# Optimization experiments

Measured on AMD Instinct MI355X. Metric: run time of the kernel, lower is better.

Reference implementation:

```python
import jax, jax.numpy as jnp
import numpy as np
import math

D_MODEL = 512
NHEAD = 8
D_K = D_MODEL // NHEAD
FACTOR = 5


def setup_inputs() -> dict:
    key = jax.random.key(0)
    ks = jax.random.split(key, 9)
    B, L = 2, 2048
    s = 1.0 / math.sqrt(D_MODEL)
    inp = {
        "x": jax.random.normal(ks[0], (B, L, D_MODEL), dtype=jnp.float32),
        "Wq": jax.random.normal(ks[1], (D_MODEL, D_MODEL), dtype=jnp.float32) * s,
        "bq": jnp.zeros((D_MODEL,), dtype=jnp.float32),
        "Wk": jax.random.normal(ks[2], (D_MODEL, D_MODEL), dtype=jnp.float32) * s,
        "bk": jnp.zeros((D_MODEL,), dtype=jnp.float32),
        "Wv": jax.random.normal(ks[3], (D_MODEL, D_MODEL), dtype=jnp.float32) * s,
        "bv": jnp.zeros((D_MODEL,), dtype=jnp.float32),
        "Wo": jax.random.normal(ks[4], (D_MODEL, D_MODEL), dtype=jnp.float32) * s,
        "bo": jnp.zeros((D_MODEL,), dtype=jnp.float32),
    }
    return inp


def reference(x, Wq, bq, Wk, bk, Wv, bv, Wo, bo):
    B, L, _ = x.shape
    # u keys kept per query (static: depends only on static L)
    u = min(L, int(FACTOR * math.log(L)) if L > 1 else L)

    def proj(W, b):
        # [B,L,D] -> [B,H,L,d_k]
        y = x @ W.T + b
        return y.reshape(B, L, NHEAD, D_K).transpose(0, 2, 1, 3)

    Q = proj(Wq, bq)
    K = proj(Wk, bk)
    V = proj(Wv, bv)

    scores = jnp.einsum("bhqd,bhkd->bhqk", Q, K) / math.sqrt(D_K)  # [B,H,L,L]
    # topk thresholding: keep only scores >= u-th largest per query row
    topk_vals, _ = jax.lax.top_k(scores, u)
    thresh = topk_vals[..., -1:]
    scores = jnp.where(scores < thresh, -10000.0, scores)
    attn = jax.nn.softmax(scores, axis=-1)  # dropout disabled (p=0 / eval)
    out = jnp.einsum("bhqk,bhkd->bhqd", attn, V)  # [B,H,L,d_k]
    out = out.transpose(0, 2, 1, 3).reshape(B, L, D_MODEL)
    return out @ Wo.T + bo
```

## Files before the change

### kernel.cpp

```cpp
#include <hip/hip_runtime.h>
#include <hip/hip_fp16.h>
#include <math.h>

#define LSEQ   2048
#define DMODEL 512
#define NHEAD  8
#define DK     64
#define UK     38

typedef __attribute__((ext_vector_type(8))) _Float16 v8h;
typedef __attribute__((ext_vector_type(4))) _Float16 v4h;
typedef __attribute__((ext_vector_type(4))) float    v4f;

__device__ __forceinline__ unsigned long long mapu64(double x){
    unsigned long long s = (unsigned long long)__double_as_longlong(x);
    return (s & 0x8000000000000000ull) ? ~s : (s | 0x8000000000000000ull);
}
__device__ __forceinline__ unsigned map32(float x){
    unsigned s = __float_as_uint(x);
    return (s & 0x80000000u) ? ~s : (s | 0x80000000u);
}
__device__ __forceinline__ float unmap32(unsigned u){
    unsigned s = (u & 0x80000000u) ? (u & 0x7fffffffu) : ~u;
    return __uint_as_float(s);
}
__device__ __forceinline__ unsigned map16(unsigned h){
    return (h & 0x8000u) ? ((~h) & 0xFFFFu) : (h | 0x8000u);
}

__global__ __launch_bounds__(256) void split_hl(
    const float* __restrict__ X,  const float* __restrict__ Wq,
    const float* __restrict__ Wk, const float* __restrict__ Wv,
    _Float16* __restrict__ Xh, _Float16* __restrict__ Xl,
    _Float16* __restrict__ Whl)
{
    const int idx = blockIdx.x * 256 + threadIdx.x;
    const int NXQ = (4096 * 512) / 4;
    const float* __restrict__ src;
    _Float16* __restrict__ dh;
    _Float16* __restrict__ dl;
    size_t off;
    if (idx < NXQ){
        src = X; dh = Xh; dl = Xl; off = (size_t)idx * 4;
    } else {
        int wi = idx - NXQ;
        int m  = wi >> 16;
        src = (m == 0) ? Wq : (m == 1 ? Wk : Wv);
        dh  = Whl + (size_t)m * 524288;
        dl  = dh + 262144;
        off = (size_t)(wi & 65535) * 4;
    }
    float4 v = *(const float4*)&src[off];
    v4h h, l;
    h[0] = (_Float16)v.x; l[0] = (_Float16)(v.x - (float)h[0]);
    h[1] = (_Float16)v.y; l[1] = (_Float16)(v.y - (float)h[1]);
    h[2] = (_Float16)v.z; l[2] = (_Float16)(v.z - (float)h[2]);
    h[3] = (_Float16)v.w; l[3] = (_Float16)(v.w - (float)h[3]);
    *(v4h*)&dh[off] = h;
    *(v4h*)&dl[off] = l;
}

__global__ __launch_bounds__(256) void qkv_f16(
    const _Float16* __restrict__ Xh, const _Float16* __restrict__ Xl,
    const _Float16* __restrict__ Whl,
    const float* __restrict__ bq, const float* __restrict__ bk,
    const float* __restrict__ bv,
    double* __restrict__ qD, double* __restrict__ kRow,
    __half* __restrict__ qH, __half* __restrict__ kH, float* __restrict__ vB)
{
    const int mode = blockIdx.z;
    const _Float16* __restrict__ Wh = Whl + (size_t)mode * 524288;
    const _Float16* __restrict__ Wl = Wh + 262144;
    const float* __restrict__ bias = (mode == 0) ? bq : (mode == 1 ? bk : bv);
    const int r0 = blockIdx.x * 64, c0 = blockIdx.y * 64;
    __shared__ _Float16 Ah[64][72], Al[64][72];
    __shared__ _Float16 Bh[64][72], Bl[64][72];
    const int tid  = threadIdx.x;
    const int lane = tid & 63, wv = tid >> 6;
    const int m0   = wv << 4;
    const int row  = lane & 15, kq = lane >> 4;

    v4f acc[4] = {};

    for (int kb = 0; kb < DMODEL; kb += 64){
        __syncthreads();
        #pragma unroll
        for (int it = 0; it < 2; ++it){
            int slot = it * 256 + tid;
            int m = slot >> 3, o8 = (slot & 7) << 3;
            size_t ga = (size_t)(r0 + m) * DMODEL + kb + o8;
            size_t gb = (size_t)(c0 + m) * DMODEL + kb + o8;
            *(v8h*)&Ah[m][o8] = *(const v8h*)&Xh[ga];
            *(v8h*)&Al[m][o8] = *(const v8h*)&Xl[ga];
            *(v8h*)&Bh[m][o8] = *(const v8h*)&Wh[gb];
            *(v8h*)&Bl[m][o8] = *(const v8h*)&Wl[gb];
        }
        __syncthreads();
        v8h ah0 = *(const v8h*)&Ah[m0 + row][kq * 8];
        v8h ah1 = *(const v8h*)&Ah[m0 + row][kq * 8 + 32];
        v8h al0 = *(const v8h*)&Al[m0 + row][kq * 8];
        v8h al1 = *(const v8h*)&Al[m0 + row][kq * 8 + 32];
        #pragma unroll
        for (int j = 0; j < 4; ++j){
            const int j0 = j << 4;
            v8h bh0 = *(const v8h*)&Bh[j0 + row][kq * 8];
            v8h bh1 = *(const v8h*)&Bh[j0 + row][kq * 8 + 32];
            v8h bl0 = *(const v8h*)&Bl[j0 + row][kq * 8];
            v8h bl1 = *(const v8h*)&Bl[j0 + row][kq * 8 + 32];
            acc[j] = __builtin_amdgcn_mfma_f32_16x16x32_f16(ah0, bh0, acc[j], 0, 0, 0);
            acc[j] = __builtin_amdgcn_mfma_f32_16x16x32_f16(ah0, bl0, acc[j], 0, 0, 0);
            acc[j] = __builtin_amdgcn_mfma_f32_16x16x32_f16(al0, bh0, acc[j], 0, 0, 0);
            acc[j] = __builtin_amdgcn_mfma_f32_16x16x32_f16(ah1, bh1, acc[j], 0, 0, 0);
            acc[j] = __builtin_amdgcn_mfma_f32_16x16x32_f16(ah1, bl1, acc[j], 0, 0, 0);
            acc[j] = __builtin_amdgcn_mfma_f32_16x16x32_f16(al1, bh1, acc[j], 0, 0, 0);
        }
    }

    const int h = c0 >> 6;
    #pragma unroll
    for (int j = 0; j < 4; ++j){
        const int dk = (j << 4) + row;
        const float bi = bias[c0 + dk];
        #pragma unroll
        for (int rr = 0; rr < 4; ++rr){
            const int r = r0 + m0 + (kq << 2) + rr;
            const int bidx = r >> 11, l = r & 2047;
            const size_t rowb = (size_t)(bidx * NHEAD + h) * LSEQ + l;
            float v = acc[j][rr] + bi;
            if (mode == 0){
                double vd = (double)v * 0.125;
                qD[rowb * DK + dk] = vd;
                ((_Float16*)qH)[rowb * DK + dk] = (_Float16)vd;
            } else if (mode == 1){
                kRow[rowb * DK + dk] = (double)v;
                ((_Float16*)kH)[rowb * DK + dk] = (_Float16)v;
            } else {
                vB[rowb * DK + dk] = v;
            }
        }
    }
}

__global__ __launch_bounds__(256) void gemm_f32(
    const float* __restrict__ X, const float* __restrict__ W,
    const float* __restrict__ bias, float* __restrict__ out)
{
    const int r0 = blockIdx.x * 64, c0 = blockIdx.y * 64;
    __shared__ float Xs[32][68];
    __shared__ float Ws[32][68];
    const int tid = threadIdx.x;
    const int tx = tid & 15, ty = tid >> 4;
    float acc[4][4] = {};
    for (int kb = 0; kb < DMODEL; kb += 32){
        __syncthreads();
        #pragma unroll
        for (int i = 0; i < 2; ++i){
            int f4 = i * 256 + tid;
            int m = f4 >> 3, kg = (f4 & 7) << 2;
            float4 xv = *(const float4*)&X[(r0 + m) * DMODEL + kb + kg];
            Xs[kg+0][m] = xv.x; Xs[kg+1][m] = xv.y; Xs[kg+2][m] = xv.z; Xs[kg+3][m] = xv.w;
            float4 wv = *(const float4*)&W[(c0 + m) * DMODEL + kb + kg];
            Ws[kg+0][m] = wv.x; Ws[kg+1][m] = wv.y; Ws[kg+2][m] = wv.z; Ws[kg+3][m] = wv.w;
        }
        __syncthreads();
        #pragma unroll
        for (int kk = 0; kk < 32; ++kk){
            float4 av = *(const float4*)&Xs[kk][ty << 2];
            float4 bv = *(const float4*)&Ws[kk][tx << 2];
            float a[4] = {av.x, av.y, av.z, av.w};
            float b[4] = {bv.x, bv.y, bv.z, bv.w};
            #pragma unroll
            for (int ii = 0; ii < 4; ++ii)
                #pragma unroll
                for (int jj = 0; jj < 4; ++jj)
                    acc[ii][jj] = fmaf(a[ii], b[jj], acc[ii][jj]);
        }
    }
    #pragma unroll
    for (int ii = 0; ii < 4; ++ii){
        int r = r0 + (ty << 2) + ii;
        float4 o;
        o.x = acc[ii][0] + bias[c0 + (tx << 2) + 0];
        o.y = acc[ii][1] + bias[c0 + (tx << 2) + 1];
        o.z = acc[ii][2] + bias[c0 + (tx << 2) + 2];
        o.w = acc[ii][3] + bias[c0 + (tx << 2) + 3];
        *(float4*)&out[(size_t)r * DMODEL + c0 + (tx << 2)] = o;
    }
}

__global__ __launch_bounds__(256) void score_gemm(
    const __half* __restrict__ qH, const __half* __restrict__ kH,
    __half* __restrict__ Sh, const int bh0)
{
    const int bh = bh0 + blockIdx.z;
    const int r0 = blockIdx.x * 64, c0 = blockIdx.y * 64;
    __shared__ _Float16 Qs[64][72];
    __shared__ _Float16 Ks[64][72];
    const int tid = threadIdx.x;
    const int lane = tid & 63, wv = tid >> 6;
    const size_t qb = ((size_t)bh * LSEQ + r0) * DK;
    const size_t kb = ((size_t)bh * LSEQ + c0) * DK;
    #pragma unroll
    for (int i = 0; i < 2; ++i){
        int c = i * 256 + tid;
        int m = c >> 3, off8 = (c & 7) << 3;
        *(v8h*)&Qs[m][off8] = *(const v8h*)&qH[qb + (size_t)m * DK + off8];
        *(v8h*)&Ks[m][off8] = *(const v8h*)&kH[kb + (size_t)m * DK + off8];
    }
    __syncthreads();
    const int m0 = wv << 4;
    const int row = lane & 15, kq = lane >> 4;
    v8h a0 = *(const v8h*)&Qs[m0 + row][kq * 8];
    v8h a1 = *(const v8h*)&Qs[m0 + row][kq * 8 + 32];
    #pragma unroll
    for (int j0 = 0; j0 < 64; j0 += 16){
        v8h b0 = *(const v8h*)&Ks[j0 + row][kq * 8];
        v8h b1 = *(const v8h*)&Ks[j0 + row][kq * 8 + 32];
        v4f acc = {0.f, 0.f, 0.f, 0.f};
        acc = __builtin_amdgcn_mfma_f32_16x16x32_f16(a0, b0, acc, 0, 0, 0);
        acc = __builtin_amdgcn_mfma_f32_16x16x32_f16(a1, b1, acc, 0, 0, 0);
        #pragma unroll
        for (int r = 0; r < 4; ++r){
            int gr = r0 + m0 + kq * 4 + r;
            int gc = c0 + j0 + row;
            Sh[((size_t)blockIdx.z * LSEQ + gr) * LSEQ + gc] = (__half)acc[r];
        }
    }
}

__device__ __forceinline__ void finish_common(
    const int ncand, const int gl, const int bh, const int lane,
    const double qd, const double* __restrict__ kRow, const float* __restrict__ vB,
    float* __restrict__ ctx, int* __restrict__ jlsR, float* __restrict__ wlsR,
    double* __restrict__ sLds)
{
    const unsigned long long mlt = (1ull << lane) - 1ull;
    if (lane >= ncand) jlsR[lane] = 0;
    if (lane < 4) jlsR[64 + lane] = 0;
    int myJ = jlsR[lane];

    double q8[8];
    #pragma unroll
    for (int k = 0; k < 8; ++k) q8[k] = __shfl(qd, (lane & 7) + (k << 3));
    const int grp = lane >> 3, dl = lane & 7;
    const size_t kb = (size_t)bh * LSEQ;
    for (int e0 = 0; e0 < ncand; e0 += 8){
        int j = jlsR[e0 + grp];
        const double* __restrict__ kr = &kRow[(kb + j) * DK + dl];
        double s = 0.0;
        #pragma unroll
        for (int k = 0; k < 8; ++k) s = fma(q8[k], kr[k << 3], s);
        s += __shfl_xor(s, 1); s += __shfl_xor(s, 2); s += __shfl_xor(s, 4);
        if (dl == 0) sLds[e0 + grp] = s;
    }
    double myS = (lane < ncand) ? sLds[lane] : -1.0e308;

    unsigned long long cu = (lane < ncand) ? mapu64(myS) : 0ull;
    unsigned long long T64 = 0ull;
    for (int bit = 63; bit >= 0; --bit){
        unsigned long long Tp = T64 | (1ull << bit);
        int c = __popcll(__ballot(cu >= Tp));
        if (c >= UK){ T64 = Tp; if (c == UK) break; }
    }
    const bool sel = (cu >= T64);

    double xm = sel ? myS : -1.0e308;
    #pragma unroll
    for (int off = 32; off; off >>= 1) xm = fmax(xm, __shfl_xor(xm, off));
    float w = sel ? expf((float)(myS - xm)) : 0.0f;
    float z = w;
    #pragma unroll
    for (int off = 32; off; off >>= 1) z += __shfl_xor(z, off);
    unsigned long long bm = __ballot(sel);
    int p = __popcll(bm & mlt);
    if (sel){ wlsR[p] = w; jlsR[p] = myJ; }
    const int cnt = __popcll(bm);
    const float invZ = 1.0f / z;

    if (lane >= cnt) wlsR[lane] = 0.0f;
    if (lane < 4){ wlsR[64 + lane] = 0.0f; jlsR[64 + lane] = 0; }

    const float* __restrict__ vsl = vB + (size_t)bh * (LSEQ * DK);
    float o = 0.0f;
    for (int e = 0; e < cnt; e += 4){
        float w0 = wlsR[e],   w1 = wlsR[e+1], w2 = wlsR[e+2], w3 = wlsR[e+3];
        int   j0 = jlsR[e],   j1 = jlsR[e+1], j2 = jlsR[e+2], j3 = jlsR[e+3];
        float v0 = vsl[(size_t)j0 * DK + lane];
        float v1 = vsl[(size_t)j1 * DK + lane];
        float v2 = vsl[(size_t)j2 * DK + lane];
        float v3 = vsl[(size_t)j3 * DK + lane];
        o = fmaf(w0, v0, o); o = fmaf(w1, v1, o);
        o = fmaf(w2, v2, o); o = fmaf(w3, v3, o);
    }
    ctx[((size_t)(bh >> 3) * LSEQ + gl) * DMODEL + (bh & 7) * DK + lane] = o * invZ;
}

__device__ __forceinline__ void finish_row_f32(
    float (&acc)[32], const int gl, const int bh, const int lane, const float margin,
    const double qd, const double* __restrict__ kRow, const float* __restrict__ vB,
    float* __restrict__ ctx, int* __restrict__ jlsR, float* __restrict__ wlsR,
    double* __restrict__ sLds)
{
    unsigned u[32];
    #pragma unroll
    for (int ch = 0; ch < 32; ++ch) u[ch] = map32(acc[ch]);
    unsigned T = 0u; int curc = 2048;
    for (int bit = 31; bit >= 0; --bit){
        unsigned Tp = T | (1u << bit);
        int c = 0;
        #pragma unroll
        for (int ch = 0; ch < 32; ++ch) c += __popcll(__ballot(u[ch] >= Tp));
        if (c >= UK){ T = Tp; curc = c; }
        if (curc <= 48) break;
    }
    const unsigned Tlo = map32(unmap32(T) - margin);
    const unsigned long long mlt = (1ull << lane) - 1ull;
    int base = 0;
    #pragma unroll
    for (int ch = 0; ch < 32; ++ch){
        bool sel = (u[ch] >= Tlo);
        unsigned long long bm = __ballot(sel);
        int p = base + __popcll(bm & mlt);
        if (sel && p < 64) jlsR[p] = (ch << 6) + lane;
        base += __popcll(bm);
    }
    const int ncand = base > 64 ? 64 : base;
    finish_common(ncand, gl, bh, lane, qd, kRow, vB, ctx, jlsR, wlsR, sLds);
}

__global__ __launch_bounds__(256) void select_kernel(
    const __half* __restrict__ Sh, const double* __restrict__ qD,
    const double* __restrict__ kRow, const float* __restrict__ vB,
    float* __restrict__ ctx, const int bh0)
{
    __shared__ int    jls[4][68];
    __shared__ float  wls[4][68];
    __shared__ double sds[4][64];
    const int tid = threadIdx.x, lane = tid & 63, wv = tid >> 6;
    const int rgS = blockIdx.x * 4 + wv;
    const int bh = bh0 + (rgS >> 11), l = rgS & 2047;
    const double qd = qD[((size_t)bh * LSEQ + l) * DK + lane];
    unsigned u[32];
    const unsigned short* __restrict__ Srow =
        (const unsigned short*)Sh + (size_t)rgS * LSEQ;
    #pragma unroll
    for (int it = 0; it < 4; ++it){
        uint4 v = *(const uint4*)&Srow[it * 512 + (lane << 3)];
        unsigned ws[4] = {v.x, v.y, v.z, v.w};
        #pragma unroll
        for (int q = 0; q < 4; ++q){
            u[it*8 + 2*q]     = map16(ws[q] & 0xFFFFu);
            u[it*8 + 2*q + 1] = map16(ws[q] >> 16);
        }
    }
    unsigned T = 0u; int curc = 2048;
    for (int bit = 15; bit >= 0; --bit){
        unsigned Tp = T | (1u << bit);
        int c = 0;
        #pragma unroll
        for (int ch = 0; ch < 32; ++ch) c += __popcll(__ballot(u[ch] >= Tp));
        if (c >= UK){ T = Tp; curc = c; }
        if (curc <= 48) break;
    }
    unsigned hb = (T & 0x8000u) ? (T & 0x7FFFu) : ((~T) & 0xFFFFu);
    float tf = __half2float(__ushort_as_half((unsigned short)hb)) - 2.2e-2f;
    unsigned short tlb = __half_as_ushort(__float2half_rd(tf));
    const unsigned Tlo = map16(tlb);

    const unsigned long long mlt = (1ull << lane) - 1ull;
    int base = 0;
    #pragma unroll
    for (int ch = 0; ch < 32; ++ch){
        bool sel = (u[ch] >= Tlo);
        unsigned long long bm = __ballot(sel);
        int p = base + __popcll(bm & mlt);
        int j = ((ch >> 3) << 9) + (lane << 3) + (ch & 7);
        if (sel && p < 64) jls[wv][p] = j;
        base += __popcll(bm);
    }
    const int ncand = base > 64 ? 64 : base;
    finish_common(ncand, l, bh, lane, qd, kRow, vB, ctx,
                  &jls[wv][0], &wls[wv][0], &sds[wv][0]);
}

__global__ __launch_bounds__(256) void attn_kernel(
    const double* __restrict__ qD, const double* __restrict__ kRow,
    const float* __restrict__ vB, float* __restrict__ ctx)
{
    __shared__ float2 Kld2[16 * 66];
    __shared__ float  qsf[8][64];
    __shared__ int    jls[8][68];
    __shared__ float  wlsf[8][68];
    __shared__ double sds[8][64];

    const int tid = threadIdx.x, lane = tid & 63, wv = tid >> 6;
    const int bh = blockIdx.x >> 8;
    const int l0 = (blockIdx.x & 255) << 3;
    const int rA = l0 + (wv << 1), rB = rA + 1;

    for (int e = tid; e < 512; e += 256){
        int r = e >> 6, d = e & 63;
        qsf[r][d] = (float)qD[((size_t)bh * LSEQ + l0 + r) * DK + d];
    }
    const double qdA = qD[((size_t)bh * LSEQ + rA) * DK + lane];
    const double qdB = qD[((size_t)bh * LSEQ + rB) * DK + lane];

    float accA[32] = {}, accB[32] = {};
    const size_t kBase = (size_t)bh * (LSEQ * DK);

    for (int dh = 0; dh < 2; ++dh){
        __syncthreads();
        float qa[32], qb[32];
        #pragma unroll
        for (int i = 0; i < 8; ++i){
            float4 va = *(const float4*)&qsf[wv << 1][dh * 32 + i * 4];
            qa[i*4+0]=va.x; qa[i*4+1]=va.y; qa[i*4+2]=va.z; qa[i*4+3]=va.w;
            float4 vb4 = *(const float4*)&qsf[(wv << 1) + 1][dh * 32 + i * 4];
            qb[i*4+0]=vb4.x; qb[i*4+1]=vb4.y; qb[i*4+2]=vb4.z; qb[i*4+3]=vb4.w;
        }
        #pragma unroll
        for (int ch = 0; ch < 32; ++ch){
            const int cb = ch << 6;
            __syncthreads();
            #pragma unroll
            for (int i = 0; i < 4; ++i){
                int j   = i * 16 + (wv << 2) + (lane >> 4);
                int dpl = lane & 15;
                double2 kd = *(const double2*)&kRow[kBase + (size_t)(cb + j) * DK + dh * 32 + dpl * 2];
                Kld2[dpl * 66 + j] = make_float2((float)kd.x, (float)kd.y);
            }
            __syncthreads();
            float a0 = accA[ch], b0 = accB[ch];
            #pragma unroll
            for (int dpl = 0; dpl < 16; ++dpl){
                float2 k = Kld2[dpl * 66 + lane];
                a0 = fmaf(qa[2*dpl],   k.x, a0);
                a0 = fmaf(qa[2*dpl+1], k.y, a0);
                b0 = fmaf(qb[2*dpl],   k.x, b0);
                b0 = fmaf(qb[2*dpl+1], k.y, b0);
            }
            accA[ch] = a0; accB[ch] = b0;
        }
    }

    finish_row_f32(accA, rA, bh, lane, 1e-3f, qdA, kRow, vB, ctx,
                   &jls[wv<<1][0], &wlsf[wv<<1][0], &sds[wv<<1][0]);
    finish_row_f32(accB, rB, bh, lane, 1e-3f, qdB, kRow, vB, ctx,
                   &jls[(wv<<1)+1][0], &wlsf[(wv<<1)+1][0], &sds[(wv<<1)+1][0]);
}

extern "C" void kernel_launch(void* const* d_in, const int* in_sizes, int n_in,
                              void* d_out, int out_size, void* d_ws, size_t ws_size,
                              hipStream_t stream)
{
    const float* x  = (const float*)d_in[0];
    const float* Wq = (const float*)d_in[1];
    const float* bq = (const float*)d_in[2];
    const float* Wk = (const float*)d_in[3];
    const float* bk = (const float*)d_in[4];
    const float* Wv = (const float*)d_in[5];
    const float* bv = (const float*)d_in[6];
    const float* Wo = (const float*)d_in[7];
    const float* bo = (const float*)d_in[8];
    float* out = (float*)d_out;
    char* ws = (char*)d_ws;
    const size_t MiB = 1024 * 1024;
    double* qD   = (double*)(ws);
    double* kRow = (double*)(ws + 16 * MiB);
    float*  vB   = (float*) (ws + 32 * MiB);
    float*  ctx  = (float*) (ws + 40 * MiB);
    __half* qH   = (__half*)(ws + 48 * MiB);
    __half* kH   = (__half*)(ws + 52 * MiB);
    __half* Sh   = (__half*)(ws + 56 * MiB);
    _Float16* Xh  = (_Float16*)(ws + 40 * MiB);
    _Float16* Xl  = (_Float16*)(ws + 44 * MiB);
    _Float16* Whl = (_Float16*)(ws + 56 * MiB);
    size_t avail = (ws_size > 56 * MiB) ? (ws_size - 56 * MiB) : 0;
    int slab = (int)(avail / (8 * MiB)); if (slab > 16) slab = 16;

    dim3 blk(256);
    split_hl<<<dim3(2816), blk, 0, stream>>>(x, Wq, Wk, Wv, Xh, Xl, Whl);
    qkv_f16 <<<dim3(64, 8, 3), blk, 0, stream>>>(Xh, Xl, Whl, bq, bk, bv,
                                                 qD, kRow, qH, kH, vB);
    if (slab >= 1){
        for (int s0 = 0; s0 < NHEAD * 2; s0 += slab){
            int nb = NHEAD * 2 - s0; if (nb > slab) nb = slab;
            score_gemm   <<<dim3(32, 32, nb), blk, 0, stream>>>(qH, kH, Sh, s0);
            select_kernel<<<dim3(nb * 512),   blk, 0, stream>>>(Sh, qD, kRow, vB, ctx, s0);
        }
    } else {
        attn_kernel<<<dim3(4096), blk, 0, stream>>>(qD, kRow, vB, ctx);
    }
    gemm_f32<<<dim3(64, 8), blk, 0, stream>>>(ctx, Wo, bo, out);
}
```

Before: 271.1 us.

## Process two query rows per wave in select kernel and pre-map score keys

```diff
diff --git a/kernel.cpp b/kernel.cpp
--- a/kernel.cpp
+++ b/kernel.cpp
@@ -223,7 +223,9 @@
         for (int r = 0; r < 4; ++r){
             int gr = r0 + m0 + kq * 4 + r;
             int gc = c0 + j0 + row;
-            Sh[((size_t)blockIdx.z * LSEQ + gr) * LSEQ + gc] = (__half)acc[r];
+            unsigned hbits = (unsigned)__half_as_ushort((__half)acc[r]);
+            unsigned short key = (unsigned short)map16(hbits);
+            ((unsigned short*)Sh)[((size_t)blockIdx.z * LSEQ + gr) * LSEQ + gc] = key;
         }
     }
 }
@@ -328,59 +330,231 @@
     finish_common(ncand, gl, bh, lane, qd, kRow, vB, ctx, jlsR, wlsR, sLds);
 }
 
+__device__ __forceinline__ void finish2(
+    const int ncA, const int ncB, const int glA, const int glB,
+    const int bh, const int lane,
+    const double* __restrict__ qD, const double* __restrict__ kRow,
+    const float* __restrict__ vB, float* __restrict__ ctx,
+    int* __restrict__ jA, float* __restrict__ wA, double* __restrict__ sdA,
+    int* __restrict__ jB, float* __restrict__ wB, double* __restrict__ sdB)
+{
+    const unsigned long long mlt = (1ull << lane) - 1ull;
+    if (lane >= ncA) jA[lane] = 0;
+    if (lane >= ncB) jB[lane] = 0;
+    if (lane < 4){ jA[64 + lane] = 0; jB[64 + lane] = 0; }
+    const int myJA = jA[lane], myJB = jB[lane];
+
+    const int grp = lane >> 3, dl = lane & 7;
+    const size_t kb = (size_t)bh * LSEQ;
+
+    double q8A[8], q8B[8];
+    {
+        const double* __restrict__ qrA = qD + (kb + glA) * DK + dl;
+        const double* __restrict__ qrB = qD + (kb + glB) * DK + dl;
+        #pragma unroll
+        for (int k = 0; k < 8; ++k){ q8A[k] = qrA[k << 3]; q8B[k] = qrB[k << 3]; }
+    }
+
+    const int pNA = (ncA + 7) >> 3, pNB = (ncB + 7) >> 3;
+    const int pN = pNA > pNB ? pNA : pNB;
+    for (int p = 0; p < pN; ++p){
+        double kvA[8], kvB[8];
+        const bool doA = (p < pNA), doB = (p < pNB);
+        if (doA){
+            int j = jA[(p << 3) + grp];
+            const double* __restrict__ kr = &kRow[(kb + j) * DK + dl];
+            #pragma unroll
+            for (int k = 0; k < 8; ++k) kvA[k] = kr[k << 3];
+        }
+        if (doB){
+            int j = jB[(p << 3) + grp];
+            const double* __restrict__ kr = &kRow[(kb + j) * DK + dl];
+            #pragma unroll
+            for (int k = 0; k < 8; ++k) kvB[k] = kr[k << 3];
+        }
+        double sA = 0.0, sB = 0.0;
+        if (doA){
+            #pragma unroll
+            for (int k = 0; k < 8; ++k) sA = fma(q8A[k], kvA[k], sA);
+        }
+        if (doB){
+            #pragma unroll
+            for (int k = 0; k < 8; ++k) sB = fma(q8B[k], kvB[k], sB);
+        }
+        sA += __shfl_xor(sA, 1); sB += __shfl_xor(sB, 1);
+        sA += __shfl_xor(sA, 2); sB += __shfl_xor(sB, 2);
+        sA += __shfl_xor(sA, 4); sB += __shfl_xor(sB, 4);
+        if (dl == 0){
+            if (doA) sdA[(p << 3) + grp] = sA;
+            if (doB) sdB[(p << 3) + grp] = sB;
+        }
+    }
+    const double mySA = (lane < ncA) ? sdA[lane] : -1.0e308;
+    const double mySB = (lane < ncB) ? sdB[lane] : -1.0e308;
+
+    const unsigned long long cuA = (lane < ncA) ? mapu64(mySA) : 0ull;
+    const unsigned long long cuB = (lane < ncB) ? mapu64(mySB) : 0ull;
+    unsigned long long TA = 0ull, TB = 0ull;
+    bool dA = false, dB = false;
+    for (int bit = 63; bit >= 0; --bit){
+        if (!dA){
+            unsigned long long Tp = TA | (1ull << bit);
+            int c = __popcll(__ballot(cuA >= Tp));
+            if (c >= UK){ TA = Tp; if (c == UK) dA = true; }
+        }
+        if (!dB){
+            unsigned long long Tp = TB | (1ull << bit);
+            int c = __popcll(__ballot(cuB >= Tp));
+            if (c >= UK){ TB = Tp; if (c == UK) dB = true; }
+        }
+        if (dA && dB) break;
+    }
+    const bool selA = (cuA >= TA), selB = (cuB >= TB);
+
+    double xmA = selA ? mySA : -1.0e308, xmB = selB ? mySB : -1.0e308;
+    #pragma unroll
+    for (int off = 32; off; off >>= 1){
+        xmA = fmax(xmA, __shfl_xor(xmA, off));
+        xmB = fmax(xmB, __shfl_xor(xmB, off));
+    }
+    float wvA = selA ? expf((float)(mySA - xmA)) : 0.0f;
+    float wvB = selB ? expf((float)(mySB - xmB)) : 0.0f;
+    float zA = wvA, zB = wvB;
+    #pragma unroll
+    for (int off = 32; off; off >>= 1){
+        zA += __shfl_xor(zA, off);
+        zB += __shfl_xor(zB, off);
+    }
+    const unsigned long long bmA = __ballot(selA), bmB = __ballot(selB);
+    const int pA = __popcll(bmA & mlt), pB = __popcll(bmB & mlt);
+    if (selA){ wA[pA] = wvA; jA[pA] = myJA; }
+    if (selB){ wB[pB] = wvB; jB[pB] = myJB; }
+    const int cntA = __popcll(bmA), cntB = __popcll(bmB);
+    const float invZA = 1.0f / zA, invZB = 1.0f / zB;
+
+    if (lane >= cntA) wA[lane] = 0.0f;
+    if (lane >= cntB) wB[lane] = 0.0f;
+    if (lane < 4){ wA[64 + lane] = 0.0f; jA[64 + lane] = 0;
+                   wB[64 + lane] = 0.0f; jB[64 + lane] = 0; }
+
+    const float* __restrict__ vsl = vB + (size_t)bh * (LSEQ * DK);
+    float oA = 0.0f, oB = 0.0f;
+    const int emax = cntA > cntB ? cntA : cntB;
+    for (int e0 = 0; e0 < emax; e0 += 16){
+        float wa16[16], va16[16]; int ja16[16];
+        float wb16[16], vb16[16]; int jb16[16];
+        const bool gA = (e0 < cntA), gB = (e0 < cntB);
+        if (gA){
+            #pragma unroll
+            for (int t = 0; t < 16; ++t){ wa16[t] = wA[e0 + t]; ja16[t] = jA[e0 + t]; }
+        }
+        if (gB){
+            #pragma unroll
+            for (int t = 0; t < 16; ++t){ wb16[t] = wB[e0 + t]; jb16[t] = jB[e0 + t]; }
+        }
+        if (gA){
+            #pragma unroll
+            for (int t = 0; t < 16; ++t) va16[t] = vsl[(size_t)ja16[t] * DK + lane];
+        }
+        if (gB){
+            #pragma unroll
+            for (int t = 0; t < 16; ++t) vb16[t] = vsl[(size_t)jb16[t] * DK + lane];
+        }
+        if (gA){
+            #pragma unroll
+            for (int t = 0; t < 16; ++t) oA = fmaf(wa16[t], va16[t], oA);
+        }
+        if (gB){
+            #pragma unroll
+            for (int t = 0; t < 16; ++t) oB = fmaf(wb16[t], vb16[t], oB);
+        }
+    }
+    const size_t cb = (size_t)(bh >> 3) * LSEQ;
+    const int hc = (bh & 7) * DK + lane;
+    ctx[(cb + glA) * DMODEL + hc] = oA * invZA;
+    ctx[(cb + glB) * DMODEL + hc] = oB * invZB;
+}
+
 __global__ __launch_bounds__(256) void select_kernel(
     const __half* __restrict__ Sh, const double* __restrict__ qD,
     const double* __restrict__ kRow, const float* __restrict__ vB,
     float* __restrict__ ctx, const int bh0)
 {
-    __shared__ int    jls[4][68];
-    __shared__ float  wls[4][68];
-    __shared__ double sds[4][64];
+    __shared__ int    jls[8][68];
+    __shared__ float  wls[8][68];
+    __shared__ double sds[8][64];
     const int tid = threadIdx.x, lane = tid & 63, wv = tid >> 6;
-    const int rgS = blockIdx.x * 4 + wv;
-    const int bh = bh0 + (rgS >> 11), l = rgS & 2047;
-    const double qd = qD[((size_t)bh * LSEQ + l) * DK + lane];
-    unsigned u[32];
-    const unsigned short* __restrict__ Srow =
-        (const unsigned short*)Sh + (size_t)rgS * LSEQ;
+    const int base = blockIdx.x * 8 + (wv << 1);
+    const int rA = base, rB = base + 1;
+    const int bh = bh0 + (rA >> 11);
+    const int glA = rA & 2047, glB = rB & 2047;
+
+    const unsigned short* __restrict__ SrA =
+        (const unsigned short*)Sh + (size_t)rA * LSEQ;
+    const unsigned short* __restrict__ SrB =
+        (const unsigned short*)Sh + (size_t)rB * LSEQ;
+    uint4 la[4], lb[4];
     #pragma unroll
     for (int it = 0; it < 4; ++it){
-        uint4 v = *(const uint4*)&Srow[it * 512 + (lane << 3)];
-        unsigned ws[4] = {v.x, v.y, v.z, v.w};
+        la[it] = *(const uint4*)&SrA[it * 512 + (lane << 3)];
+        lb[it] = *(const uint4*)&SrB[it * 512 + (lane << 3)];
+    }
+    unsigned uA[32], uB[32];
+    #pragma unroll
+    for (int it = 0; it < 4; ++it){
+        unsigned wsA[4] = {la[it].x, la[it].y, la[it].z, la[it].w};
+        unsigned wsB[4] = {lb[it].x, lb[it].y, lb[it].z, lb[it].w};
         #pragma unroll
         for (int q = 0; q < 4; ++q){
-            u[it*8 + 2*q]     = map16(ws[q] & 0xFFFFu);
-            u[it*8 + 2*q + 1] = map16(ws[q] >> 16);
-        }
-    }
-    unsigned T = 0u; int curc = 2048;
+            uA[it*8 + 2*q]     = wsA[q] & 0xFFFFu;
+            uA[it*8 + 2*q + 1] = wsA[q] >> 16;
+            uB[it*8 + 2*q]     = wsB[q] & 0xFFFFu;
+            uB[it*8 + 2*q + 1] = wsB[q] >> 16;
+        }
+    }
+
+    unsigned TA = 0u, TB = 0u;
     for (int bit = 15; bit >= 0; --bit){
-        unsigned Tp = T | (1u << bit);
-        int c = 0;
-        #pragma unroll
-        for (int ch = 0; ch < 32; ++ch) c += __popcll(__ballot(u[ch] >= Tp));
-        if (c >= UK){ T = Tp; curc = c; }
-        if (curc <= 48) break;
-    }
-    unsigned hb = (T & 0x8000u) ? (T & 0x7FFFu) : ((~T) & 0xFFFFu);
-    float tf = __half2float(__ushort_as_half((unsigned short)hb)) - 2.2e-2f;
-    unsigned short tlb = __half_as_ushort(__float2half_rd(tf));
-    const unsigned Tlo = map16(tlb);
+        const unsigned TpA = TA | (1u << bit), TpB = TB | (1u << bit);
+        int cA = 0, cB = 0;
+        #pragma unroll
+        for (int ch = 0; ch < 32; ++ch){
+            cA += __popcll(__ballot(uA[ch] >= TpA));
+            cB += __popcll(__ballot(uB[ch] >= TpB));
+        }
+        if (cA >= UK) TA = TpA;
+        if (cB >= UK) TB = TpB;
+    }
+    unsigned hbA = (TA & 0x8000u) ? (TA & 0x7FFFu) : ((~TA) & 0xFFFFu);
+    unsigned hbB = (TB & 0x8000u) ? (TB & 0x7FFFu) : ((~TB) & 0xFFFFu);
+    float tfA = __half2float(__ushort_as_half((unsigned short)hbA)) - 2.2e-2f;
+    float tfB = __half2float(__ushort_as_half((unsigned short)hbB)) - 2.2e-2f;
+    const unsigned TloA = map16(__half_as_ushort(__float2half_rd(tfA)));
+    const unsigned TloB = map16(__half_as_ushort(__float2half_rd(tfB)));
 
     const unsigned long long mlt = (1ull << lane) - 1ull;
-    int base = 0;
+    int baseA = 0, baseB = 0;
+    int* __restrict__ jA = &jls[wv << 1][0];
+    int* __restrict__ jB = &jls[(wv << 1) + 1][0];
     #pragma unroll
     for (int ch = 0; ch < 32; ++ch){
-        bool sel = (u[ch] >= Tlo);
-        unsigned long long bm = __ballot(sel);
-        int p = base + __popcll(bm & mlt);
-        int j = ((ch >> 3) << 9) + (lane << 3) + (ch & 7);
-        if (sel && p < 64) jls[wv][p] = j;
-        base += __popcll(bm);
-    }
-    const int ncand = base > 64 ? 64 : base;
-    finish_common(ncand, l, bh, lane, qd, kRow, vB, ctx,
-                  &jls[wv][0], &wls[wv][0], &sds[wv][0]);
+        const int j = ((ch >> 3) << 9) + (lane << 3) + (ch & 7);
+        const bool sA = (uA[ch] >= TloA);
+        const bool sB = (uB[ch] >= TloB);
+        const unsigned long long bmA = __ballot(sA);
+        const unsigned long long bmB = __ballot(sB);
+        const int pA = baseA + __popcll(bmA & mlt);
+        const int pB = baseB + __popcll(bmB & mlt);
+        if (sA && pA < 64) jA[pA] = j;
+        if (sB && pB < 64) jB[pB] = j;
+        baseA += __popcll(bmA);
+        baseB += __popcll(bmB);
+    }
+    const int ncA = baseA > 64 ? 64 : baseA;
+    const int ncB = baseB > 64 ? 64 : baseB;
+    finish2(ncA, ncB, glA, glB, bh, lane, qD, kRow, vB, ctx,
+            jA, &wls[wv << 1][0], &sds[wv << 1][0],
+            jB, &wls[(wv << 1) + 1][0], &sds[(wv << 1) + 1][0]);
 }
 
 __global__ __launch_bounds__(256) void attn_kernel(
@@ -486,7 +660,7 @@
         for (int s0 = 0; s0 < NHEAD * 2; s0 += slab){
             int nb = NHEAD * 2 - s0; if (nb > slab) nb = slab;
             score_gemm   <<<dim3(32, 32, nb), blk, 0, stream>>>(qH, kH, Sh, s0);
-            select_kernel<<<dim3(nb * 512),   blk, 0, stream>>>(Sh, qD, kRow, vB, ctx, s0);
+            select_kernel<<<dim3(nb * 256),   blk, 0, stream>>>(Sh, qD, kRow, vB, ctx, s0);
         }
     } else {
         attn_kernel<<<dim3(4096), blk, 0, stream>>>(qD, kRow, vB, ctx);
```

Measured after the change: 309.6 us. +14.2%, slower.

## Compute scores in split-fp16 precision and skip double-precision refinement when threshold is clear

Applied to the files above, without the earlier changes.

```diff
diff --git a/kernel.cpp b/kernel.cpp
--- a/kernel.cpp
+++ b/kernel.cpp
@@ -23,9 +23,6 @@
 __device__ __forceinline__ float unmap32(unsigned u){
     unsigned s = (u & 0x80000000u) ? (u & 0x7fffffffu) : ~u;
     return __uint_as_float(s);
-}
-__device__ __forceinline__ unsigned map16(unsigned h){
-    return (h & 0x8000u) ? ((~h) & 0xFFFFu) : (h | 0x8000u);
 }
 
 __global__ __launch_bounds__(256) void split_hl(
@@ -66,7 +63,9 @@
     const float* __restrict__ bq, const float* __restrict__ bk,
     const float* __restrict__ bv,
     double* __restrict__ qD, double* __restrict__ kRow,
-    __half* __restrict__ qH, __half* __restrict__ kH, float* __restrict__ vB)
+    _Float16* __restrict__ qH, _Float16* __restrict__ kH,
+    _Float16* __restrict__ qL, _Float16* __restrict__ kL,
+    float* __restrict__ vB)
 {
     const int mode = blockIdx.z;
     const _Float16* __restrict__ Wh = Whl + (size_t)mode * 524288;
@@ -130,10 +129,15 @@
             if (mode == 0){
                 double vd = (double)v * 0.125;
                 qD[rowb * DK + dk] = vd;
-                ((_Float16*)qH)[rowb * DK + dk] = (_Float16)vd;
+                float sf = (float)vd;
+                _Float16 hi = (_Float16)sf;
+                qH[rowb * DK + dk] = hi;
+                qL[rowb * DK + dk] = (_Float16)(sf - (float)hi);
             } else if (mode == 1){
                 kRow[rowb * DK + dk] = (double)v;
-                ((_Float16*)kH)[rowb * DK + dk] = (_Float16)v;
+                _Float16 hi = (_Float16)v;
+                kH[rowb * DK + dk] = hi;
+                kL[rowb * DK + dk] = (_Float16)(v - (float)hi);
             } else {
                 vB[rowb * DK + dk] = v;
             }
@@ -189,13 +193,14 @@
 }
 
 __global__ __launch_bounds__(256) void score_gemm(
-    const __half* __restrict__ qH, const __half* __restrict__ kH,
-    __half* __restrict__ Sh, const int bh0)
+    const _Float16* __restrict__ qH, const _Float16* __restrict__ qL,
+    const _Float16* __restrict__ kH, const _Float16* __restrict__ kL,
+    unsigned* __restrict__ Sk, const int bh0)
 {
     const int bh = bh0 + blockIdx.z;
     const int r0 = blockIdx.x * 64, c0 = blockIdx.y * 64;
-    __shared__ _Float16 Qs[64][72];
-    __shared__ _Float16 Ks[64][72];
+    __shared__ _Float16 Qh[64][72], Ql[64][72];
+    __shared__ _Float16 Kh[64][72], Kl[64][72];
     const int tid = threadIdx.x;
     const int lane = tid & 63, wv = tid >> 6;
     const size_t qb = ((size_t)bh * LSEQ + r0) * DK;
@@ -204,26 +209,38 @@
     for (int i = 0; i < 2; ++i){
         int c = i * 256 + tid;
         int m = c >> 3, off8 = (c & 7) << 3;
-        *(v8h*)&Qs[m][off8] = *(const v8h*)&qH[qb + (size_t)m * DK + off8];
-        *(v8h*)&Ks[m][off8] = *(const v8h*)&kH[kb + (size_t)m * DK + off8];
+        size_t qa = qb + (size_t)m * DK + off8;
+        size_t ka = kb + (size_t)m * DK + off8;
+        *(v8h*)&Qh[m][off8] = *(const v8h*)&qH[qa];
+        *(v8h*)&Ql[m][off8] = *(const v8h*)&qL[qa];
+        *(v8h*)&Kh[m][off8] = *(const v8h*)&kH[ka];
+        *(v8h*)&Kl[m][off8] = *(const v8h*)&kL[ka];
     }
     __syncthreads();
     const int m0 = wv << 4;
     const int row = lane & 15, kq = lane >> 4;
-    v8h a0 = *(const v8h*)&Qs[m0 + row][kq * 8];
-    v8h a1 = *(const v8h*)&Qs[m0 + row][kq * 8 + 32];
+    v8h a0h = *(const v8h*)&Qh[m0 + row][kq * 8];
+    v8h a1h = *(const v8h*)&Qh[m0 + row][kq * 8 + 32];
+    v8h a0l = *(const v8h*)&Ql[m0 + row][kq * 8];
+    v8h a1l = *(const v8h*)&Ql[m0 + row][kq * 8 + 32];
     #pragma unroll
     for (int j0 = 0; j0 < 64; j0 += 16){
-        v8h b0 = *(const v8h*)&Ks[j0 + row][kq * 8];
-        v8h b1 = *(const v8h*)&Ks[j0 + row][kq * 8 + 32];
+        v8h b0h = *(const v8h*)&Kh[j0 + row][kq * 8];
+        v8h b1h = *(const v8h*)&Kh[j0 + row][kq * 8 + 32];
+        v8h b0l = *(const v8h*)&Kl[j0 + row][kq * 8];
+        v8h b1l = *(const v8h*)&Kl[j0 + row][kq * 8 + 32];
         v4f acc = {0.f, 0.f, 0.f, 0.f};
-        acc = __builtin_amdgcn_mfma_f32_16x16x32_f16(a0, b0, acc, 0, 0, 0);
-        acc = __builtin_amdgcn_mfma_f32_16x16x32_f16(a1, b1, acc, 0, 0, 0);
+        acc = __builtin_amdgcn_mfma_f32_16x16x32_f16(a0h, b0l, acc, 0, 0, 0);
+        acc = __builtin_amdgcn_mfma_f32_16x16x32_f16(a1h, b1l, acc, 0, 0, 0);
+        acc = __builtin_amdgcn_mfma_f32_16x16x32_f16(a0l, b0h, acc, 0, 0, 0);
+        acc = __builtin_amdgcn_mfma_f32_16x16x32_f16(a1l, b1h, acc, 0, 0, 0);
+        acc = __builtin_amdgcn_mfma_f32_16x16x32_f16(a0h, b0h, acc, 0, 0, 0);
+        acc = __builtin_amdgcn_mfma_f32_16x16x32_f16(a1h, b1h, acc, 0, 0, 0);
         #pragma unroll
         for (int r = 0; r < 4; ++r){
             int gr = r0 + m0 + kq * 4 + r;
             int gc = c0 + j0 + row;
-            Sh[((size_t)blockIdx.z * LSEQ + gr) * LSEQ + gc] = (__half)acc[r];
+            Sk[((size_t)blockIdx.z * LSEQ + gr) * LSEQ + gc] = map32(acc[r]);
         }
     }
 }
@@ -329,58 +346,115 @@
 }
 
 __global__ __launch_bounds__(256) void select_kernel(
-    const __half* __restrict__ Sh, const double* __restrict__ qD,
+    const unsigned* __restrict__ Sk, const double* __restrict__ qD,
     const double* __restrict__ kRow, const float* __restrict__ vB,
     float* __restrict__ ctx, const int bh0)
 {
-    __shared__ int    jls[4][68];
-    __shared__ float  wls[4][68];
-    __shared__ double sds[4][64];
+    __shared__ int      jls[4][68];
+    __shared__ float    wls[4][68];
+    __shared__ unsigned kls[4][68];
+    __shared__ double   sds[4][64];
     const int tid = threadIdx.x, lane = tid & 63, wv = tid >> 6;
     const int rgS = blockIdx.x * 4 + wv;
     const int bh = bh0 + (rgS >> 11), l = rgS & 2047;
-    const double qd = qD[((size_t)bh * LSEQ + l) * DK + lane];
+    const unsigned* __restrict__ Srow = Sk + (size_t)rgS * LSEQ;
+
     unsigned u[32];
-    const unsigned short* __restrict__ Srow =
-        (const unsigned short*)Sh + (size_t)rgS * LSEQ;
     #pragma unroll
     for (int it = 0; it < 4; ++it){
-        uint4 v = *(const uint4*)&Srow[it * 512 + (lane << 3)];
-        unsigned ws[4] = {v.x, v.y, v.z, v.w};
-        #pragma unroll
-        for (int q = 0; q < 4; ++q){
-            u[it*8 + 2*q]     = map16(ws[q] & 0xFFFFu);
-            u[it*8 + 2*q + 1] = map16(ws[q] >> 16);
-        }
-    }
-    unsigned T = 0u; int curc = 2048;
-    for (int bit = 15; bit >= 0; --bit){
+        uint4 va = *(const uint4*)&Srow[it * 512 + (lane << 3)];
+        uint4 vb = *(const uint4*)&Srow[it * 512 + (lane << 3) + 4];
+        u[it*8+0] = va.x; u[it*8+1] = va.y; u[it*8+2] = va.z; u[it*8+3] = va.w;
+        u[it*8+4] = vb.x; u[it*8+5] = vb.y; u[it*8+6] = vb.z; u[it*8+7] = vb.w;
+    }
+
+    unsigned T = 0u; bool done = false;
+    for (int bit = 31; bit >= 0 && !done; --bit){
         unsigned Tp = T | (1u << bit);
         int c = 0;
         #pragma unroll
         for (int ch = 0; ch < 32; ++ch) c += __popcll(__ballot(u[ch] >= Tp));
-        if (c >= UK){ T = Tp; curc = c; }
-        if (curc <= 48) break;
-    }
-    unsigned hb = (T & 0x8000u) ? (T & 0x7FFFu) : ((~T) & 0xFFFFu);
-    float tf = __half2float(__ushort_as_half((unsigned short)hb)) - 2.2e-2f;
-    unsigned short tlb = __half_as_ushort(__float2half_rd(tf));
-    const unsigned Tlo = map16(tlb);
+        if (c >= UK){ T = Tp; if (c == UK) done = true; }
+    }
+
+    unsigned m39 = 0u;
+    #pragma unroll
+    for (int ch = 0; ch < 32; ++ch){
+        unsigned uv = u[ch];
+        if (uv < T && uv > m39) m39 = uv;
+    }
+    #pragma unroll
+    for (int off = 32; off; off >>= 1){
+        unsigned o = (unsigned)__shfl_xor((int)m39, off);
+        if (o > m39) m39 = o;
+    }
 
     const unsigned long long mlt = (1ull << lane) - 1ull;
+    int* __restrict__      jR = &jls[wv][0];
+    float* __restrict__    wR = &wls[wv][0];
+    unsigned* __restrict__ kR = &kls[wv][0];
     int base = 0;
+    #pragma unroll
+    for (int ch = 0; ch < 32; ++ch){
+        bool sel = (u[ch] >= T);
+        unsigned long long bm = __ballot(sel);
+        int p = base + __popcll(bm & mlt);
+        if (sel && p < 64){
+            jR[p] = ((ch >> 3) << 9) + (lane << 3) + (ch & 7);
+            kR[p] = u[ch];
+        }
+        base += __popcll(bm);
+    }
+    const int cnt = base;
+    const float gap = unmap32(T) - unmap32(m39);
+
+    if (cnt == UK && gap > 1e-4f){
+        if (lane >= cnt) jR[lane] = 0;
+        if (lane < 4){ jR[64 + lane] = 0; wR[64 + lane] = 0.0f; }
+        unsigned myk = (lane < cnt) ? kR[lane] : 0u;
+        unsigned km = myk;
+        #pragma unroll
+        for (int off = 32; off; off >>= 1){
+            unsigned o = (unsigned)__shfl_xor((int)km, off);
+            km = km > o ? km : o;
+        }
+        const float smax = unmap32(km);
+        float w = (lane < cnt) ? expf(unmap32(myk) - smax) : 0.0f;
+        wR[lane] = w;
+        float z = w;
+        #pragma unroll
+        for (int off = 32; off; off >>= 1) z += __shfl_xor(z, off);
+        const float invZ = 1.0f / z;
+
+        const float* __restrict__ vsl = vB + (size_t)bh * (LSEQ * DK);
+        float o = 0.0f;
+        for (int e = 0; e < cnt; e += 4){
+            float w0 = wR[e],   w1 = wR[e+1], w2 = wR[e+2], w3 = wR[e+3];
+            int   j0 = jR[e],   j1 = jR[e+1], j2 = jR[e+2], j3 = jR[e+3];
+            float v0 = vsl[(size_t)j0 * DK + lane];
+            float v1 = vsl[(size_t)j1 * DK + lane];
+            float v2 = vsl[(size_t)j2 * DK + lane];
+            float v3 = vsl[(size_t)j3 * DK + lane];
+            o = fmaf(w0, v0, o); o = fmaf(w1, v1, o);
+            o = fmaf(w2, v2, o); o = fmaf(w3, v3, o);
+        }
+        ctx[((size_t)(bh >> 3) * LSEQ + l) * DMODEL + (bh & 7) * DK + lane] = o * invZ;
+        return;
+    }
+
+    const double qd = qD[((size_t)bh * LSEQ + l) * DK + lane];
+    const unsigned Tlo = map32(unmap32(T) - 1e-3f);
+    base = 0;
     #pragma unroll
     for (int ch = 0; ch < 32; ++ch){
         bool sel = (u[ch] >= Tlo);
         unsigned long long bm = __ballot(sel);
         int p = base + __popcll(bm & mlt);
-        int j = ((ch >> 3) << 9) + (lane << 3) + (ch & 7);
-        if (sel && p < 64) jls[wv][p] = j;
+        if (sel && p < 64) jR[p] = ((ch >> 3) << 9) + (lane << 3) + (ch & 7);
         base += __popcll(bm);
     }
     const int ncand = base > 64 ? 64 : base;
-    finish_common(ncand, l, bh, lane, qd, kRow, vB, ctx,
-                  &jls[wv][0], &wls[wv][0], &sds[wv][0]);
+    finish_common(ncand, l, bh, lane, qd, kRow, vB, ctx, jR, wR, &sds[wv][0]);
 }
 
 __global__ __launch_bounds__(256) void attn_kernel(
@@ -465,28 +539,30 @@
     float* out = (float*)d_out;
     char* ws = (char*)d_ws;
     const size_t MiB = 1024 * 1024;
-    double* qD   = (double*)(ws);
-    double* kRow = (double*)(ws + 16 * MiB);
-    float*  vB   = (float*) (ws + 32 * MiB);
-    float*  ctx  = (float*) (ws + 40 * MiB);
-    __half* qH   = (__half*)(ws + 48 * MiB);
-    __half* kH   = (__half*)(ws + 52 * MiB);
-    __half* Sh   = (__half*)(ws + 56 * MiB);
-    _Float16* Xh  = (_Float16*)(ws + 40 * MiB);
-    _Float16* Xl  = (_Float16*)(ws + 44 * MiB);
-    _Float16* Whl = (_Float16*)(ws + 56 * MiB);
-    size_t avail = (ws_size > 56 * MiB) ? (ws_size - 56 * MiB) : 0;
-    int slab = (int)(avail / (8 * MiB)); if (slab > 16) slab = 16;
+    double*   qD   = (double*)  (ws);
+    double*   kRow = (double*)  (ws + 16 * MiB);
+    float*    vB   = (float*)   (ws + 32 * MiB);
+    float*    ctx  = (float*)   (ws + 40 * MiB);
+    _Float16* qH   = (_Float16*)(ws + 48 * MiB);
+    _Float16* kH   = (_Float16*)(ws + 52 * MiB);
+    _Float16* qL   = (_Float16*)(ws + 56 * MiB);
+    _Float16* kL   = (_Float16*)(ws + 60 * MiB);
+    unsigned* Sk   = (unsigned*)(ws + 64 * MiB);
+    _Float16* Xh   = (_Float16*)(ws + 40 * MiB);
+    _Float16* Xl   = (_Float16*)(ws + 44 * MiB);
+    _Float16* Whl  = (_Float16*)(ws + 64 * MiB);
+    size_t avail = (ws_size > 64 * MiB) ? (ws_size - 64 * MiB) : 0;
+    int slab = (int)(avail / (16 * MiB)); if (slab > 16) slab = 16;
 
     dim3 blk(256);
     split_hl<<<dim3(2816), blk, 0, stream>>>(x, Wq, Wk, Wv, Xh, Xl, Whl);
     qkv_f16 <<<dim3(64, 8, 3), blk, 0, stream>>>(Xh, Xl, Whl, bq, bk, bv,
-                                                 qD, kRow, qH, kH, vB);
+                                                 qD, kRow, qH, kH, qL, kL, vB);
     if (slab >= 1){
         for (int s0 = 0; s0 < NHEAD * 2; s0 += slab){
             int nb = NHEAD * 2 - s0; if (nb > slab) nb = slab;
-            score_gemm   <<<dim3(32, 32, nb), blk, 0, stream>>>(qH, kH, Sh, s0);
-            select_kernel<<<dim3(nb * 512),   blk, 0, stream>>>(Sh, qD, kRow, vB, ctx, s0);
+            score_gemm   <<<dim3(32, 32, nb), blk, 0, stream>>>(qH, qL, kH, kL, Sk, s0);
+            select_kernel<<<dim3(nb * 512),   blk, 0, stream>>>(Sk, qD, kRow, vB, ctx, s0);
         }
     } else {
         attn_kernel<<<dim3(4096), blk, 0, stream>>>(qD, kRow, vB, ctx);
```

Measured after the change: 369.3 us. 36.2% more time.
